# Kernel optimization log

Measured on AMD Instinct MI355X. Metric: run time of the kernel, lower is better.

The kernel has to match this reference:

```python
import jax, jax.numpy as jnp
import numpy as np

N = 100000
E = 1600000
D = 128      # input_dim == hidden_dim
C = 40       # output_dim
L = 3        # num_layers
EPS = 1e-12  # F.normalize eps


def setup_inputs() -> dict:
    key = jax.random.key(0)
    ks = jax.random.split(key, 8)
    x = jax.random.normal(ks[0], (N, D), dtype=jnp.float32)
    edge_index = jax.random.randint(ks[1], (2, E), 0, N, dtype=jnp.int64)
    s = 1.0 / np.sqrt(D)
    # SAGEConv: lin_l (neighbor path, with bias), lin_r (root path, no bias)
    Wl = jax.random.uniform(ks[2], (L, D, D), jnp.float32, -s, s)
    bl = jax.random.uniform(ks[3], (L, D), jnp.float32, -s, s)
    Wr = jax.random.uniform(ks[4], (L, D, D), jnp.float32, -s, s)
    Wlin = jax.random.uniform(ks[5], (C, D), jnp.float32, -s, s)
    blin = jax.random.uniform(ks[6], (C,), jnp.float32, -s, s)
    return {"x": x, "edge_index": edge_index, "Wl": Wl, "bl": bl,
            "Wr": Wr, "Wlin": Wlin, "blin": blin}


def reference(x, edge_index, Wl, bl, Wr, Wlin, blin):
    src, dst = edge_index[0], edge_index[1]
    # in-degree counts for mean aggregation (computed once, reused per layer)
    cnt = jax.ops.segment_sum(jnp.ones((E,), jnp.float32), dst, num_segments=N)
    inv_cnt = (1.0 / jnp.maximum(cnt, 1.0))[:, None]  # [N,1]
    z = x
    for i in range(L):
        msg = z[src]  # gather [E, D]
        agg = jax.ops.segment_sum(msg, dst, num_segments=N) * inv_cnt  # mean [N, D]
        out = agg @ Wl[i].T + bl[i] + z @ Wr[i].T
        # SAGEConv normalize=True: L2 normalize per node
        nrm = jnp.linalg.norm(out, axis=-1, keepdims=True)
        out = out / jnp.maximum(nrm, EPS)
        z = jax.nn.relu(out)  # dropout p=0 -> identity
    return z @ Wlin.T + blin  # [N, C]
```

## Files before the change

kernel.cpp:

```cpp
#include <hip/hip_runtime.h>


typedef __bf16 bf16x8 __attribute__((ext_vector_type(8)));
typedef float  f32x4  __attribute__((ext_vector_type(4)));

#define MFMA16(a, b, c) __builtin_amdgcn_mfma_f32_16x16x32_bf16((a), (b), (c), 0, 0, 0)

__device__ __forceinline__ unsigned rne_bf16(float f) {
  unsigned u = __float_as_uint(f);
  unsigned r = u + 0x7FFFu + ((u >> 16) & 1u);
  return r >> 16;
}

__device__ __forceinline__ float bf_lo(unsigned u) { return __uint_as_float(u << 16); }
__device__ __forceinline__ float bf_hi(unsigned u) { return __uint_as_float(u & 0xFFFF0000u); }

__device__ __forceinline__ void gload_lds16(const void* g, void* l) {
  __builtin_amdgcn_global_load_lds(
      (const __attribute__((address_space(1))) unsigned int*)g,
      (__attribute__((address_space(3))) unsigned int*)l, 16, 0, 0);
}

__global__ __launch_bounds__(256) void prep_k(
    const float* __restrict__ x, const float* __restrict__ Wl,
    const float* __restrict__ Wr, const float* __restrict__ Wlin,
    uint2* __restrict__ planeA, unsigned short* __restrict__ wfrag,
    unsigned short* __restrict__ wlf, int* __restrict__ gcur,
    int cap, int n4) {
  const int b = blockIdx.x;
  const int tid = threadIdx.x;
  if (b == 0) {
    if (tid < 128) gcur[tid] = tid * cap;
    return;
  }
  if (b <= 96) {
    int id = (b - 1) * 256 + tid;
    int l = id & 63;
    int c = (id >> 6) & 7;
    int t = (id >> 9) & 7;
    int p = (id >> 12) & 1;
    int layer = id >> 13;
    int col = t * 16 + (l & 15);
    int kbase = c * 32 + (l >> 4) * 8;
    unsigned short* dst = wfrag + (size_t)layer * 65536 +
                          ((((size_t)p * 8 + t) * 8 + c) * 64 + l) * 8;
#pragma unroll
    for (int j = 0; j < 8; ++j) {
      int k = kbase + j;
      float w = (k < 128) ? Wl[layer * 16384 + col * 128 + k]
                          : Wr[layer * 16384 + col * 128 + (k - 128)];
      unsigned h = rne_bf16(w);
      unsigned o;
      if (p == 0) o = h;
      else o = rne_bf16(w - __uint_as_float(h << 16));
      dst[j] = (unsigned short)o;
    }
    return;
  }
  if (b == 97) {
    for (int id = tid; id < 3 * 4 * 64; id += 256) {
      int l = id & 63;
      int c = (id >> 6) & 3;
      int t = id >> 8;
      int col = t * 16 + (l & 15);
      int kbase = c * 32 + (l >> 4) * 8;
      unsigned short* dst = wlf + (size_t)id * 8;
#pragma unroll
      for (int j = 0; j < 8; ++j) {
        float w = (col < 40) ? Wlin[col * 128 + kbase + j] : 0.f;
        dst[j] = (unsigned short)rne_bf16(w);
      }
    }
    return;
  }
  int i = (b - 98) * 256 + tid;
  if (i >= n4) return;
  float4 f = ((const float4*)x)[i];
  uint2 o;
  o.x = rne_bf16(f.x) | (rne_bf16(f.y) << 16);
  o.y = rne_bf16(f.z) | (rne_bf16(f.w) << 16);
  planeA[i] = o;
}


__global__ __launch_bounds__(256) void bucketA_k(
    const int* __restrict__ src, const int* __restrict__ dst,
    int* __restrict__ gcur, unsigned* __restrict__ coarse, int E, int nc) {
  __shared__ int hist[128];
  __shared__ int sd[128];
  __shared__ int lpos[128];
  __shared__ int gbase[128];
  __shared__ unsigned stage[2048];
  __shared__ unsigned char sbuck[2048];

  const int tid = threadIdx.x;
  const int e0 = blockIdx.x * 2048;

  if (tid < 128) hist[tid] = 0;
  __syncthreads();

  int bv[8], pk[8];
#pragma unroll
  for (int j = 0; j < 8; ++j) {
    int e = e0 + j * 256 + tid;
    bv[j] = -1;
    if (e < E) {
      int s = src[e], d = dst[e];
      bv[j] = d >> 10;
      pk[j] = s | ((d & 1023) << 17);
      atomicAdd(&hist[bv[j]], 1);
    }
  }
  __syncthreads();

  if (tid < 128) sd[tid] = hist[tid];
  __syncthreads();
  for (int off = 1; off < 128; off <<= 1) {
    int t = 0;
    if (tid < 128 && tid >= off) t = sd[tid - off];
    __syncthreads();
    if (tid < 128) sd[tid] += t;
    __syncthreads();
  }
  if (tid < 128) {
    int excl = sd[tid] - hist[tid];
    lpos[tid] = excl;
    gbase[tid] = (tid < nc && hist[tid] > 0) ? atomicAdd(&gcur[tid], hist[tid]) : 0;
  }
  __syncthreads();

#pragma unroll
  for (int j = 0; j < 8; ++j) {
    if (bv[j] >= 0) {
      int slot = atomicAdd(&lpos[bv[j]], 1);
      stage[slot] = (unsigned)pk[j];
      sbuck[slot] = (unsigned char)bv[j];
    }
  }
  __syncthreads();

  const int total = sd[127];
  for (int i = tid; i < total; i += 256) {
    int b = sbuck[i];
    int excl = sd[b] - hist[b];
    coarse[gbase[b] + (i - excl)] = stage[i];
  }
}

__global__ __launch_bounds__(256) void bucketB_k(
    const int* __restrict__ gcur, const unsigned* __restrict__ coarse, int cap,
    int* __restrict__ esrc, int* __restrict__ offsets,
    float* __restrict__ inv_cnt, int n, int nc) {
  __shared__ int hcnt[1024];
  __shared__ int cur[1024];
  __shared__ int sd[256];
  __shared__ int sh_gdst;

  const int tid = threadIdx.x;
  const int b = blockIdx.x;
  const int base = b * 1024;
  const int nn = (n - base < 1024) ? (n - base) : 1024;
  const int wbeg = b * cap;
  const int wend = gcur[b];

  if (tid < 128) {
    int v = (tid < nc) ? (gcur[tid] - tid * cap) : 0;
    sd[tid] = v;
  }
  __syncthreads();
  for (int off = 1; off < 128; off <<= 1) {
    int u = 0;
    if (tid < 128 && tid >= off) u = sd[tid - off];
    __syncthreads();
    if (tid < 128) sd[tid] += u;
    __syncthreads();
  }
  if (tid == b) sh_gdst = sd[tid] - (wend - wbeg);
  for (int j = tid; j < 1024; j += 256) hcnt[j] = 0;
  __syncthreads();
  const int gdst = sh_gdst;

  for (int idx = wbeg + tid; idx < wend; idx += 256)
    atomicAdd(&hcnt[coarse[idx] >> 17], 1);
  __syncthreads();

  int b0 = hcnt[tid * 4], b1 = hcnt[tid * 4 + 1];
  int b2 = hcnt[tid * 4 + 2], b3 = hcnt[tid * 4 + 3];
  int tot = b0 + b1 + b2 + b3;
  sd[tid] = tot;
  __syncthreads();
  for (int off = 1; off < 256; off <<= 1) {
    int u = (tid >= off) ? sd[tid - off] : 0;
    __syncthreads();
    sd[tid] += u;
    __syncthreads();
  }
  int excl = gdst + sd[tid] - tot;
  cur[tid * 4]     = excl;
  cur[tid * 4 + 1] = excl + b0;
  cur[tid * 4 + 2] = excl + b0 + b1;
  cur[tid * 4 + 3] = excl + b0 + b1 + b2;
  __syncthreads();

  for (int j = tid; j < nn; j += 256) {
    offsets[base + j] = cur[j];
    int c = hcnt[j] > 1 ? hcnt[j] : 1;
    inv_cnt[base + j] = 1.0f / (float)c;
  }
  if (tid == 0 && base + nn >= n) offsets[n] = gdst + (wend - wbeg);
  __syncthreads();

  for (int idx = wbeg + tid; idx < wend; idx += 256) {
    unsigned p = coarse[idx];
    int pos = atomicAdd(&cur[p >> 17], 1);
    esrc[pos] = (int)(p & 0x1FFFFu);
  }
}

__global__ void aggregate_k(const unsigned short* __restrict__ zb,
                            const int* __restrict__ offsets,
                            const int* __restrict__ esrc,
                            const float* __restrict__ inv_cnt,
                            unsigned short* __restrict__ aggh, int n) {
  int node = (blockIdx.x * 256 + threadIdx.x) >> 4;
  int l16 = threadIdx.x & 15;
  if (node >= n) return;
  int beg = offsets[node], end = offsets[node + 1];
  float a0 = 0.f, a1 = 0.f, a2 = 0.f, a3 = 0.f;
  float a4 = 0.f, a5 = 0.f, a6 = 0.f, a7 = 0.f;
  int t = beg;
  for (; t + 4 <= end; t += 4) {
    int s0 = esrc[t], s1 = esrc[t + 1], s2 = esrc[t + 2], s3 = esrc[t + 3];
    uint4 d0 = *(const uint4*)(zb + (size_t)s0 * 128 + l16 * 8);
    uint4 d1 = *(const uint4*)(zb + (size_t)s1 * 128 + l16 * 8);
    uint4 d2 = *(const uint4*)(zb + (size_t)s2 * 128 + l16 * 8);
    uint4 d3 = *(const uint4*)(zb + (size_t)s3 * 128 + l16 * 8);
    a0 += bf_lo(d0.x); a1 += bf_hi(d0.x); a2 += bf_lo(d0.y); a3 += bf_hi(d0.y);
    a4 += bf_lo(d0.z); a5 += bf_hi(d0.z); a6 += bf_lo(d0.w); a7 += bf_hi(d0.w);
    a0 += bf_lo(d1.x); a1 += bf_hi(d1.x); a2 += bf_lo(d1.y); a3 += bf_hi(d1.y);
    a4 += bf_lo(d1.z); a5 += bf_hi(d1.z); a6 += bf_lo(d1.w); a7 += bf_hi(d1.w);
    a0 += bf_lo(d2.x); a1 += bf_hi(d2.x); a2 += bf_lo(d2.y); a3 += bf_hi(d2.y);
    a4 += bf_lo(d2.z); a5 += bf_hi(d2.z); a6 += bf_lo(d2.w); a7 += bf_hi(d2.w);
    a0 += bf_lo(d3.x); a1 += bf_hi(d3.x); a2 += bf_lo(d3.y); a3 += bf_hi(d3.y);
    a4 += bf_lo(d3.z); a5 += bf_hi(d3.z); a6 += bf_lo(d3.w); a7 += bf_hi(d3.w);
  }
  for (; t + 2 <= end; t += 2) {
    int s0 = esrc[t], s1 = esrc[t + 1];
    uint4 d0 = *(const uint4*)(zb + (size_t)s0 * 128 + l16 * 8);
    uint4 d1 = *(const uint4*)(zb + (size_t)s1 * 128 + l16 * 8);
    a0 += bf_lo(d0.x); a1 += bf_hi(d0.x); a2 += bf_lo(d0.y); a3 += bf_hi(d0.y);
    a4 += bf_lo(d0.z); a5 += bf_hi(d0.z); a6 += bf_lo(d0.w); a7 += bf_hi(d0.w);
    a0 += bf_lo(d1.x); a1 += bf_hi(d1.x); a2 += bf_lo(d1.y); a3 += bf_hi(d1.y);
    a4 += bf_lo(d1.z); a5 += bf_hi(d1.z); a6 += bf_lo(d1.w); a7 += bf_hi(d1.w);
  }
  if (t < end) {
    int s0 = esrc[t];
    uint4 d0 = *(const uint4*)(zb + (size_t)s0 * 128 + l16 * 8);
    a0 += bf_lo(d0.x); a1 += bf_hi(d0.x); a2 += bf_lo(d0.y); a3 += bf_hi(d0.y);
    a4 += bf_lo(d0.z); a5 += bf_hi(d0.z); a6 += bf_lo(d0.w); a7 += bf_hi(d0.w);
  }
  float ic = inv_cnt[node];
  uint4 hv;
  hv.x = rne_bf16(a0 * ic) | (rne_bf16(a1 * ic) << 16);
  hv.y = rne_bf16(a2 * ic) | (rne_bf16(a3 * ic) << 16);
  hv.z = rne_bf16(a4 * ic) | (rne_bf16(a5 * ic) << 16);
  hv.w = rne_bf16(a6 * ic) | (rne_bf16(a7 * ic) << 16);
  *(uint4*)(aggh + (size_t)node * 128 + l16 * 8) = hv;
}

template <bool FUSE>
__global__ __launch_bounds__(256) void sage_layer_mfma_k(
    const unsigned short* __restrict__ zb, const unsigned short* __restrict__ aggh,
    const unsigned short* __restrict__ wf, const float* __restrict__ bl,
    unsigned short* __restrict__ out_bf,
    const unsigned short* __restrict__ wlf, const float* __restrict__ blin,
    float* __restrict__ fout, int n, int ntiles) {
  __shared__ unsigned short Ah_s[2][32 * 256];
  __shared__ unsigned short Zt_s[FUSE ? 32 * 128 : 8];
  __shared__ float psum[2][2][4][16];

  const int lane = threadIdx.x & 63;
  const int wv = threadIdx.x >> 6;
  const int g = lane >> 4;
  const int rl = lane & 15;

  const bf16x8* wfv = (const bf16x8*)wf;
  const int t0 = wv * 2, t1 = wv * 2 + 1;
  bf16x8 Bh0[8], Bh1[8], Bl0[8], Bl1[8];
#pragma unroll
  for (int c = 0; c < 8; ++c) {
    Bh0[c] = wfv[((0 * 8 + t0) * 8 + c) * 64 + lane];
    Bh1[c] = wfv[((0 * 8 + t1) * 8 + c) * 64 + lane];
    Bl0[c] = wfv[((1 * 8 + t0) * 8 + c) * 64 + lane];
    Bl1[c] = wfv[((1 * 8 + t1) * 8 + c) * 64 + lane];
  }
  const float b0 = bl[t0 * 16 + rl];
  const float b1 = bl[t1 * 16 + rl];

  char* pZt = (char*)Zt_s;
  const bf16x8* wlfv = (const bf16x8*)wlf;

  const int rsub = lane >> 5;
  const int hlf = (lane >> 4) & 1;
  const int b16 = lane & 15;

  int tile = blockIdx.x;
  if (tile >= ntiles) return;

  {
    const int v0 = tile * 32;
#pragma unroll
    for (int q = 0; q < 4; ++q) {
      int wq = wv * 4 + q;
      int r = wq * 2 + rsub;
      int v = v0 + r; v = (v < n) ? v : (n - 1);
      int sblk = b16 ^ (r & 7);
      gload_lds16((hlf ? zb : aggh) + (size_t)v * 128 + sblk * 8,
                  (char*)Ah_s[0] + wq * 1024);
    }
  }
  __syncthreads();

  int cur = 0, par = 0;
  while (tile < ntiles) {
    const int next = tile + gridDim.x;
    if (next < ntiles) {
      const int v0n = next * 32;
#pragma unroll
      for (int q = 0; q < 4; ++q) {
        int wq = wv * 4 + q;
        int r = wq * 2 + rsub;
        int v = v0n + r; v = (v < n) ? v : (n - 1);
        int sblk = b16 ^ (r & 7);
        gload_lds16((hlf ? zb : aggh) + (size_t)v * 128 + sblk * 8,
                    (char*)Ah_s[cur ^ 1] + wq * 1024);
      }
    }

    const int v0 = tile * 32;
    char* pAh = (char*)Ah_s[cur];

    f32x4 a00 = {0.f,0.f,0.f,0.f}, a10 = {0.f,0.f,0.f,0.f};
    f32x4 a01 = {0.f,0.f,0.f,0.f}, a11 = {0.f,0.f,0.f,0.f};
    {
      const int swz = (rl & 7) << 4;
      const int row0 = rl * 512;
      const int row1 = (16 + rl) * 512;
#pragma unroll
      for (int c = 0; c < 8; ++c) {
        int o0 = (row0 + c * 64 + g * 16) ^ swz;
        int o1 = (row1 + c * 64 + g * 16) ^ swz;
        bf16x8 ah0 = *(const bf16x8*)(pAh + o0);
        bf16x8 ah1 = *(const bf16x8*)(pAh + o1);
        a00 = MFMA16(ah0, Bh0[c], a00); a10 = MFMA16(ah0, Bh1[c], a10);
        a00 = MFMA16(ah0, Bl0[c], a00); a10 = MFMA16(ah0, Bl1[c], a10);
        a01 = MFMA16(ah1, Bh0[c], a01); a11 = MFMA16(ah1, Bh1[c], a11);
        a01 = MFMA16(ah1, Bl0[c], a01); a11 = MFMA16(ah1, Bl1[c], a11);
      }
    }

    {
      float pr0[4], pr1[4];
#pragma unroll
      for (int j = 0; j < 4; ++j) {
        a00[j] += b0; a10[j] += b1;
        a01[j] += b0; a11[j] += b1;
        pr0[j] = a00[j]*a00[j] + a10[j]*a10[j];
        pr1[j] = a01[j]*a01[j] + a11[j]*a11[j];
      }
#pragma unroll
      for (int m = 1; m < 16; m <<= 1) {
#pragma unroll
        for (int j = 0; j < 4; ++j) {
          pr0[j] += __shfl_xor(pr0[j], m);
          pr1[j] += __shfl_xor(pr1[j], m);
        }
      }
      if (rl == 0) {
#pragma unroll
        for (int j = 0; j < 4; ++j) {
          psum[par][0][wv][g * 4 + j] = pr0[j];
          psum[par][1][wv][g * 4 + j] = pr1[j];
        }
      }
    }
    __syncthreads();

#pragma unroll
    for (int s = 0; s < 2; ++s) {
      f32x4& A0 = s ? a01 : a00;
      f32x4& A1 = s ? a11 : a10;
#pragma unroll
      for (int j = 0; j < 4; ++j) {
        int row16 = g * 4 + j;
        float tot = psum[par][s][0][row16] + psum[par][s][1][row16] +
                    psum[par][s][2][row16] + psum[par][s][3][row16];
        float inv = 1.0f / fmaxf(sqrtf(tot), 1e-12f);
        int v = v0 + s * 16 + row16;
        float o0 = fmaxf(A0[j] * inv, 0.f);
        float o1 = fmaxf(A1[j] * inv, 0.f);
        unsigned short q0 = (unsigned short)rne_bf16(o0);
        unsigned short q1 = (unsigned short)rne_bf16(o1);
        if (!FUSE) {
          if (v < n) {
            out_bf[(size_t)v * 128 + t0 * 16 + rl] = q0;
            out_bf[(size_t)v * 128 + t1 * 16 + rl] = q1;
          }
        } else {
          int rloc = s * 16 + row16;
          int sw = (rloc & 7) << 4;
          *(unsigned short*)(pZt + ((rloc * 256 + (t0 * 16 + rl) * 2) ^ sw)) = q0;
          *(unsigned short*)(pZt + ((rloc * 256 + (t1 * 16 + rl) * 2) ^ sw)) = q1;
        }
      }
    }

    if (FUSE) {
      __syncthreads();
      for (int job = wv; job < 6; job += 4) {
        int s = job / 3, t = job % 3;
        f32x4 acc = {0.f, 0.f, 0.f, 0.f};
        const int rowz = s * 16 + rl;
        const int swzz = (rowz & 7) << 4;
#pragma unroll
        for (int c = 0; c < 4; ++c) {
          bf16x8 a = *(const bf16x8*)(pZt + ((rowz * 256 + c * 64 + g * 16) ^ swzz));
          bf16x8 bw = wlfv[(t * 4 + c) * 64 + lane];
          acc = MFMA16(a, bw, acc);
        }
        int col = t * 16 + rl;
        if (col < 40) {
          float bb = blin[col];
#pragma unroll
          for (int j = 0; j < 4; ++j) {
            int v = v0 + s * 16 + g * 4 + j;
            if (v < n) fout[(size_t)v * 40 + col] = acc[j] + bb;
          }
        }
      }
      __syncthreads();
    }

    tile = next; cur ^= 1; par ^= 1;
  }
}


extern "C" void kernel_launch(void* const* d_in, const int* in_sizes, int n_in,
                              void* d_out, int out_size, void* d_ws, size_t ws_size,
                              hipStream_t stream) {
  const float* x    = (const float*)d_in[0];
  const int*   ei   = (const int*)d_in[1];
  const float* Wl   = (const float*)d_in[2];
  const float* bl   = (const float*)d_in[3];
  const float* Wr   = (const float*)d_in[4];
  const float* Wlin = (const float*)d_in[5];
  const float* blin = (const float*)d_in[6];

  const int N = in_sizes[0] / 128;
  const int E = in_sizes[1] / 2;
  const int D = 128;
  const int NC = (N + 1023) >> 10;
  const int cap = (E + NC - 1) / NC + 4096;

  const int* src = ei;
  const int* dstp = ei + E;

  unsigned short* planeA = (unsigned short*)d_ws;
  unsigned short* planeB = planeA + (size_t)N * D;
  unsigned short* aggh   = planeB + (size_t)N * D;
  float* inv_cnt = (float*)(aggh + (size_t)N * D);
  unsigned short* wlf = (unsigned short*)(inv_cnt + N);
  unsigned short* Wfrag = wlf + 6144;
  int*   offsets = (int*)(Wfrag + 3 * 65536);
  int*   esrc    = offsets + N + 1;
  unsigned* coarse = (unsigned*)(esrc + E);
  int*   gcur    = (int*)(coarse + (size_t)NC * cap);

  const int n4 = N * 32;
  prep_k<<<98 + (n4 + 255) / 256, 256, 0, stream>>>(
      x, Wl, Wr, Wlin, (uint2*)planeA, Wfrag, wlf, gcur, cap, n4);

  bucketA_k<<<(E + 2047) / 2048, 256, 0, stream>>>(src, dstp, gcur, coarse, E, NC);
  bucketB_k<<<NC, 256, 0, stream>>>(gcur, coarse, cap, esrc, offsets, inv_cnt, N, NC);

  const int aggGrid = (N * 16 + 255) / 256;
  const int ntiles = (N + 31) / 32;
  const int sageGrid = 768;

  aggregate_k<<<aggGrid, 256, 0, stream>>>(planeA, offsets, esrc, inv_cnt, aggh, N);
  sage_layer_mfma_k<false><<<sageGrid, 256, 0, stream>>>(
      planeA, aggh, Wfrag + 0 * 65536, bl + 0 * D, planeB, wlf, blin, nullptr, N, ntiles);
  aggregate_k<<<aggGrid, 256, 0, stream>>>(planeB, offsets, esrc, inv_cnt, aggh, N);
  sage_layer_mfma_k<false><<<sageGrid, 256, 0, stream>>>(
      planeB, aggh, Wfrag + 1 * 65536, bl + 1 * D, planeA, wlf, blin, nullptr, N, ntiles);
  aggregate_k<<<aggGrid, 256, 0, stream>>>(planeA, offsets, esrc, inv_cnt, aggh, N);
  sage_layer_mfma_k<true><<<sageGrid, 256, 0, stream>>>(
      planeA, aggh, Wfrag + 2 * 65536, bl + 2 * D, nullptr, wlf, blin,
      (float*)d_out, N, ntiles);
}
```

Before: 366.1 us.

## Drop low-order weight correction on root path and simplify tile loop

The two-term (hi/lo) bf16 weight split is kept only for the aggregated-neighbour half of the K dimension. The root-path half now uses only the high-order weights, which removes a quarter of the MFMAs and frees registers, at some cost in accuracy. The double-buffered LDS prefetch of the next tile is replaced by a single buffer that is loaded and then synchronised each iteration. The end-of-iteration barrier is removed, and the persistent grid grows from 768 to 1024 blocks. Without that barrier, the next tile's LDS loads may overwrite data other waves are still reading.

```diff
diff --git a/kernel.cpp b/kernel.cpp
--- a/kernel.cpp
+++ b/kernel.cpp
@@ -275,7 +275,7 @@
     unsigned short* __restrict__ out_bf,
     const unsigned short* __restrict__ wlf, const float* __restrict__ blin,
     float* __restrict__ fout, int n, int ntiles) {
-  __shared__ unsigned short Ah_s[2][32 * 256];
+  __shared__ unsigned short Ah_s[32 * 256];
   __shared__ unsigned short Zt_s[FUSE ? 32 * 128 : 8];
   __shared__ float psum[2][2][4][16];
 
@@ -286,17 +286,21 @@
 
   const bf16x8* wfv = (const bf16x8*)wf;
   const int t0 = wv * 2, t1 = wv * 2 + 1;
-  bf16x8 Bh0[8], Bh1[8], Bl0[8], Bl1[8];
+  bf16x8 Bh0[8], Bh1[8], Bl0[4], Bl1[4];
 #pragma unroll
   for (int c = 0; c < 8; ++c) {
     Bh0[c] = wfv[((0 * 8 + t0) * 8 + c) * 64 + lane];
     Bh1[c] = wfv[((0 * 8 + t1) * 8 + c) * 64 + lane];
+  }
+#pragma unroll
+  for (int c = 0; c < 4; ++c) {
     Bl0[c] = wfv[((1 * 8 + t0) * 8 + c) * 64 + lane];
     Bl1[c] = wfv[((1 * 8 + t1) * 8 + c) * 64 + lane];
   }
   const float b0 = bl[t0 * 16 + rl];
   const float b1 = bl[t1 * 16 + rl];
 
+  char* pAh = (char*)Ah_s;
   char* pZt = (char*)Zt_s;
   const bf16x8* wlfv = (const bf16x8*)wlf;
 
@@ -304,41 +308,21 @@
   const int hlf = (lane >> 4) & 1;
   const int b16 = lane & 15;
 
-  int tile = blockIdx.x;
-  if (tile >= ntiles) return;
-
-  {
+  int par = 0;
+  for (int tile = blockIdx.x; tile < ntiles; tile += gridDim.x) {
     const int v0 = tile * 32;
+
 #pragma unroll
     for (int q = 0; q < 4; ++q) {
       int wq = wv * 4 + q;
       int r = wq * 2 + rsub;
       int v = v0 + r; v = (v < n) ? v : (n - 1);
       int sblk = b16 ^ (r & 7);
-      gload_lds16((hlf ? zb : aggh) + (size_t)v * 128 + sblk * 8,
-                  (char*)Ah_s[0] + wq * 1024);
-    }
-  }
-  __syncthreads();
-
-  int cur = 0, par = 0;
-  while (tile < ntiles) {
-    const int next = tile + gridDim.x;
-    if (next < ntiles) {
-      const int v0n = next * 32;
-#pragma unroll
-      for (int q = 0; q < 4; ++q) {
-        int wq = wv * 4 + q;
-        int r = wq * 2 + rsub;
-        int v = v0n + r; v = (v < n) ? v : (n - 1);
-        int sblk = b16 ^ (r & 7);
-        gload_lds16((hlf ? zb : aggh) + (size_t)v * 128 + sblk * 8,
-                    (char*)Ah_s[cur ^ 1] + wq * 1024);
-      }
-    }
-
-    const int v0 = tile * 32;
-    char* pAh = (char*)Ah_s[cur];
+      const unsigned short* srcp =
+          (hlf ? zb : aggh) + (size_t)v * 128 + sblk * 8;
+      gload_lds16(srcp, pAh + wq * 1024);
+    }
+    __syncthreads();
 
     f32x4 a00 = {0.f,0.f,0.f,0.f}, a10 = {0.f,0.f,0.f,0.f};
     f32x4 a01 = {0.f,0.f,0.f,0.f}, a11 = {0.f,0.f,0.f,0.f};
@@ -347,7 +331,7 @@
       const int row0 = rl * 512;
       const int row1 = (16 + rl) * 512;
 #pragma unroll
-      for (int c = 0; c < 8; ++c) {
+      for (int c = 0; c < 4; ++c) {
         int o0 = (row0 + c * 64 + g * 16) ^ swz;
         int o1 = (row1 + c * 64 + g * 16) ^ swz;
         bf16x8 ah0 = *(const bf16x8*)(pAh + o0);
@@ -356,6 +340,15 @@
         a00 = MFMA16(ah0, Bl0[c], a00); a10 = MFMA16(ah0, Bl1[c], a10);
         a01 = MFMA16(ah1, Bh0[c], a01); a11 = MFMA16(ah1, Bh1[c], a11);
         a01 = MFMA16(ah1, Bl0[c], a01); a11 = MFMA16(ah1, Bl1[c], a11);
+      }
+#pragma unroll
+      for (int c = 4; c < 8; ++c) {
+        int o0 = (row0 + c * 64 + g * 16) ^ swz;
+        int o1 = (row1 + c * 64 + g * 16) ^ swz;
+        bf16x8 ah0 = *(const bf16x8*)(pAh + o0);
+        bf16x8 ah1 = *(const bf16x8*)(pAh + o1);
+        a00 = MFMA16(ah0, Bh0[c], a00); a10 = MFMA16(ah0, Bh1[c], a10);
+        a01 = MFMA16(ah1, Bh0[c], a01); a11 = MFMA16(ah1, Bh1[c], a11);
       }
     }
 
@@ -438,10 +431,8 @@
           }
         }
       }
-      __syncthreads();
-    }
-
-    tile = next; cur ^= 1; par ^= 1;
+    }
+    par ^= 1;
   }
 }
 
@@ -486,7 +477,7 @@
 
   const int aggGrid = (N * 16 + 255) / 256;
   const int ntiles = (N + 31) / 32;
-  const int sageGrid = 768;
+  const int sageGrid = 1024;
 
   aggregate_k<<<aggGrid, 256, 0, stream>>>(planeA, offsets, esrc, inv_cnt, aggh, N);
   sage_layer_mfma_k<false><<<sageGrid, 256, 0, stream>>>(
```

Measured after the change: 348.2 us. 4.9% less time.
